# Optimization experiments

Measured on AMD Instinct MI355X. Metric: run time of the kernel, lower is better.

## Reference

```python
import jax, jax.numpy as jnp
import numpy as np

NUM_HEADS = 8
DIMS = 512
SR = 2
EPS = 1e-6


def setup_inputs() -> dict:
    key = jax.random.key(0)
    ks = jax.random.split(key, 12)
    B, H, W, C = 4, 64, 64, DIMS
    s = 0.02
    return {
        "x": jax.random.normal(ks[0], (B, H * W, C), dtype=jnp.float32),
        "Wq": jax.random.normal(ks[1], (C, DIMS), dtype=jnp.float32) * s,
        "bq": jnp.zeros((DIMS,), jnp.float32),
        "Wk": jax.random.normal(ks[2], (C, DIMS), dtype=jnp.float32) * s,
        "bk": jnp.zeros((DIMS,), jnp.float32),
        "Wv": jax.random.normal(ks[3], (C, DIMS), dtype=jnp.float32) * s,
        "bv": jnp.zeros((DIMS,), jnp.float32),
        "Wp": jax.random.normal(ks[4], (DIMS, DIMS), dtype=jnp.float32) * s,
        "bp": jnp.zeros((DIMS,), jnp.float32),
        "sr_w": jax.random.normal(ks[5], (SR, SR, C, DIMS), dtype=jnp.float32) * s,  # HWIO
        "sr_b": jnp.zeros((DIMS,), jnp.float32),
        "ln_g": jnp.ones((DIMS,), jnp.float32),
        "ln_b": jnp.zeros((DIMS,), jnp.float32),
        "H": 64,
        "W": 64,
    }


def reference(x, Wq, bq, Wk, bk, Wv, bv, Wp, bp, sr_w, sr_b, ln_g, ln_b, H, W):
    B, N, C = x.shape
    hd = DIMS // NUM_HEADS

    # spatial-reduction of K/V: strided conv (kernel=stride=SR, SAME) + LayerNorm
    kv = x.reshape(B, H, W, C)
    kv = jax.lax.conv_general_dilated(
        kv, sr_w, window_strides=(SR, SR), padding="SAME",
        dimension_numbers=("NHWC", "HWIO", "NHWC")) + sr_b
    kv = kv.reshape(B, -1, C)  # [B, Nk, C], Nk = (H//SR)*(W//SR)
    mu = jnp.mean(kv, axis=-1, keepdims=True)
    var = jnp.mean(jnp.square(kv - mu), axis=-1, keepdims=True)
    kv = (kv - mu) * jax.lax.rsqrt(var + EPS) * ln_g + ln_b
    Nk = kv.shape[1]

    # NOTE: original splits heads as reshape(B, N, head_dims, num_heads) and
    # indexes the LAST axis per head -> head h sees channels d*NUM_HEADS+h.
    q = (x @ Wq + bq).reshape(B, N, hd, NUM_HEADS)
    k = (kv @ Wk + bk).reshape(B, Nk, hd, NUM_HEADS)
    v = (kv @ Wv + bv).reshape(B, Nk, hd, NUM_HEADS)

    scores = jnp.einsum("bqdh,bkdh->bhqk", q, k) / jnp.sqrt(jnp.float32(hd))
    w = jax.nn.softmax(scores, axis=-1)
    # concat of heads along channels -> (B, N, NUM_HEADS, hd) layout
    out = jnp.einsum("bhqk,bkdh->bqhd", w, v).reshape(B, N, DIMS)
    return out @ Wp + bp
```

## Files before the change

### kernel.cpp

```cpp
#include <hip/hip_runtime.h>


typedef __attribute__((ext_vector_type(8))) _Float16 f16x8;
typedef __attribute__((ext_vector_type(4))) _Float16 f16x4;
typedef __attribute__((ext_vector_type(4))) float f32x4;

#define EXP2F(x) __builtin_amdgcn_exp2f(x)

__device__ __forceinline__ void gload_lds16(const _Float16* g, _Float16* l)
{
    __builtin_amdgcn_global_load_lds(
        (const __attribute__((address_space(1))) void*)g,
        (__attribute__((address_space(3))) void*)l, 16, 0, 0);
}

template<int N>
__device__ __forceinline__ void wait_vm()
{
    asm volatile("s_waitcnt vmcnt(%0)" :: "n"(N) : "memory");
}

__global__ __launch_bounds__(256)
void prep_k(const float* __restrict__ x,
            const float* __restrict__ Wq, const float* __restrict__ Wk,
            const float* __restrict__ Wv, const float* __restrict__ Wp,
            const float* __restrict__ srw,
            _Float16* __restrict__ xh, _Float16* __restrict__ wqt,
            _Float16* __restrict__ wkvt, _Float16* __restrict__ wpt,
            _Float16* __restrict__ srwt)
{
    __shared__ float T[32][33];
    const int id = blockIdx.x;
    const int t = threadIdx.x;

    if (id < 4096) {
        const size_t i = ((size_t)id * 256 + t) * 8;
        const float4 a = *(const float4*)(x + i);
        const float4 b = *(const float4*)(x + i + 4);
        f16x8 o;
        o[0] = (_Float16)a.x; o[1] = (_Float16)a.y; o[2] = (_Float16)a.z; o[3] = (_Float16)a.w;
        o[4] = (_Float16)b.x; o[5] = (_Float16)b.y; o[6] = (_Float16)b.z; o[7] = (_Float16)b.w;
        *(f16x8*)(xh + i) = o;
        return;
    }

    if (id < 5120) {
        const int id2 = id - 4096;
        const int z = id2 >> 8, k0 = ((id2 >> 4) & 15) * 32, n0 = (id2 & 15) * 32;
        const float* src; _Float16* dst; int perm;
        switch (z) {
            case 0:  src = Wq; dst = wqt;           perm = 1; break;
            case 1:  src = Wk; dst = wkvt;          perm = 1; break;
            case 2:  src = Wv; dst = wkvt + 262144; perm = 0; break;
            default: src = Wp; dst = wpt;           perm = 0; break;
        }
        {
            const int r = t >> 3, c = (t & 7) * 4;
            const float4 v = *(const float4*)(src + (size_t)(k0 + r) * 512 + n0 + c);
            T[r][c + 0] = v.x; T[r][c + 1] = v.y; T[r][c + 2] = v.z; T[r][c + 3] = v.w;
        }
        __syncthreads();
        {
            const int j = t >> 3, i0 = (t & 7) * 4;
            const int n = n0 + j;
            const int nper = perm ? ((n & 7) * 64 + (n >> 3)) : n;
            f16x4 o;
            o[0] = (_Float16)T[i0 + 0][j];
            o[1] = (_Float16)T[i0 + 1][j];
            o[2] = (_Float16)T[i0 + 2][j];
            o[3] = (_Float16)T[i0 + 3][j];
            *(f16x4*)(dst + (size_t)nper * 512 + k0 + i0) = o;
        }
        return;
    }

    {
        const int id3 = id - 5120;
        const int n0 = (id3 & 15) * 32, k0 = (id3 >> 4) * 32;
        {
            const int r = t >> 3, c = (t & 7) * 4;
            const float4 v = *(const float4*)(srw + (size_t)(k0 + r) * 512 + n0 + c);
            T[r][c + 0] = v.x; T[r][c + 1] = v.y; T[r][c + 2] = v.z; T[r][c + 3] = v.w;
        }
        __syncthreads();
        {
            const int j = t >> 3, i0 = (t & 7) * 4;
            f16x4 o;
            o[0] = (_Float16)T[i0 + 0][j];
            o[1] = (_Float16)T[i0 + 1][j];
            o[2] = (_Float16)T[i0 + 2][j];
            o[3] = (_Float16)T[i0 + 3][j];
            *(f16x4*)(srwt + (size_t)(n0 + j) * 2048 + k0 + i0) = o;
        }
        return;
    }
}

template<int MODE, bool CONV, int BM>
__device__ __forceinline__ void gemm_body(
    const int bx, const int by,
    const _Float16* __restrict__ A, const _Float16* __restrict__ Wt,
    const float* __restrict__ bias, const float* __restrict__ bias2,
    void* __restrict__ Cv, void* __restrict__ Cv2,
    _Float16* __restrict__ As, _Float16* __restrict__ Ws)
{
    constexpr int K = CONV ? 2048 : 512;
    constexpr int NIT = K / 32;
    constexpr int MT = BM / 32;
    constexpr int AI = BM / 64;
    constexpr int ABUF = BM * 32;
    constexpr int NBUF = (BM == 64) ? 4 : 3;
    constexpr int P = NBUF - 1;
    constexpr int L = AI + 2;
    const int tid = threadIdx.x;
    const int wave = tid >> 6, lane = tid & 63;
    const int quad = lane >> 4, l15 = lane & 15;
    const int wm = wave >> 1, wn = wave & 1;
    const int wrow = wm * (BM / 2);
    const int m0 = by * BM, n0 = bx * 128;

    const _Float16* abase[AI];
    int ac8[AI];
    #pragma unroll
    for (int t = 0; t < AI; ++t) {
        const int e = (wave * AI + t) * 64 + lane;
        const int row = e >> 2, c8 = (e & 3) * 8;
        ac8[t] = c8;
        if (CONV) {
            const int grow = m0 + row;
            const int b = grow >> 10, rem = grow & 1023;
            const int oh = rem >> 5, ow = rem & 31;
            abase[t] = A + ((size_t)((b * 64 + 2 * oh) * 64) + 2 * ow) * 512;
        } else {
            abase[t] = A + (size_t)(m0 + row) * K + c8;
        }
    }
    const _Float16* wbase[2];
    #pragma unroll
    for (int t = 0; t < 2; ++t) {
        const int e = (wave * 2 + t) * 64 + lane;
        const int row = e >> 2, c8 = (e & 3) * 8;
        wbase[t] = Wt + (size_t)(n0 + row) * K + c8;
    }

    auto stage = [&](const int k0, const int buf) {
        #pragma unroll
        for (int t = 0; t < AI; ++t) {
            const _Float16* gp;
            if (CONV) {
                const int gk = k0 + ac8[t];
                gp = abase[t] + ((gk >> 10) & 1) * 32768 + ((gk >> 9) & 1) * 512
                              + (gk & 511);
            } else {
                gp = abase[t] + k0;
            }
            gload_lds16(gp, &As[buf * ABUF + (wave * AI + t) * 512]);
        }
        #pragma unroll
        for (int t = 0; t < 2; ++t)
            gload_lds16(wbase[t] + k0, &Ws[buf * 4096 + (wave * 2 + t) * 512]);
    };

    f32x4 acc[MT][4] = {};

    #pragma unroll
    for (int p = 0; p < P; ++p) stage(p * 32, p);

    int cur = 0, nxt = P % NBUF;
    for (int it = 0; it < NIT; ++it) {
        int rem = NIT - 1 - it;
        if (rem > P - 1) rem = P - 1;
        switch (rem) {
            case 0:  wait_vm<0>(); break;
            case 1:  wait_vm<L>(); break;
            case 2:  wait_vm<2 * L>(); break;
            default: wait_vm<3 * L>(); break;
        }
        __builtin_amdgcn_s_barrier();
        __builtin_amdgcn_sched_barrier(0);
        if (it + P < NIT) {
            stage((it + P) * 32, nxt);
            nxt = (nxt + 1 == NBUF) ? 0 : nxt + 1;
        }

        f16x8 af[MT], bf[4];
        #pragma unroll
        for (int mt = 0; mt < MT; ++mt)
            af[mt] = *(const f16x8*)&As[cur * ABUF + (wrow + mt * 16 + l15) * 32 + quad * 8];
        #pragma unroll
        for (int nt = 0; nt < 4; ++nt)
            bf[nt] = *(const f16x8*)&Ws[cur * 4096 + (wn * 64 + nt * 16 + l15) * 32 + quad * 8];
        #pragma unroll
        for (int mt = 0; mt < MT; ++mt)
            #pragma unroll
            for (int nt = 0; nt < 4; ++nt)
                acc[mt][nt] = __builtin_amdgcn_mfma_f32_16x16x32_f16(
                    af[mt], bf[nt], acc[mt][nt], 0, 0, 0);

        cur = (cur + 1 == NBUF) ? 0 : cur + 1;
    }

    #pragma unroll
    for (int nt = 0; nt < 4; ++nt) {
        const int gcol = n0 + wn * 64 + nt * 16 + l15;
        float bv;
        if (MODE == 6) bv = bias[(gcol & 63) * 8 + (gcol >> 6)];
        else if (MODE == 5) bv = (gcol < 512) ? bias[(gcol & 63) * 8 + (gcol >> 6)]
                                              : bias2[gcol - 512];
        else bv = bias[gcol];
        #pragma unroll
        for (int mt = 0; mt < MT; ++mt) {
            const int row0 = m0 + wrow + mt * 16 + quad * 4;
            if (MODE == 0) {
                #pragma unroll
                for (int r = 0; r < 4; ++r)
                    ((float*)Cv)[(size_t)(row0 + r) * 512 + gcol] = acc[mt][nt][r] + bv;
            } else if (MODE == 4 || MODE == 6) {
                #pragma unroll
                for (int r = 0; r < 4; ++r)
                    ((_Float16*)Cv)[(size_t)(row0 + r) * 512 + gcol] =
                        (_Float16)(acc[mt][nt][r] + bv);
            } else {
                if (gcol < 512) {
                    #pragma unroll
                    for (int r = 0; r < 4; ++r)
                        ((_Float16*)Cv)[(size_t)(row0 + r) * 512 + gcol] =
                            (_Float16)(acc[mt][nt][r] + bv);
                } else {
                    const int c = gcol - 512;
                    const int h = c & 7, d = c >> 3;
                    const int b_ = row0 >> 10, jj = row0 & 1023;
                    f16x4 o;
                    #pragma unroll
                    for (int r = 0; r < 4; ++r) o[r] = (_Float16)(acc[mt][nt][r] + bv);
                    *(f16x4*)((_Float16*)Cv2 +
                              ((size_t)(b_ * 8 + h) * 64 + d) * 1024 + jj) = o;
                }
            }
        }
    }
}

template<int MODE, bool CONV, int BM>
__global__ __launch_bounds__(256)
void gemm_f16(const _Float16* __restrict__ A, const _Float16* __restrict__ Wt,
              const float* __restrict__ bias, const float* __restrict__ bias2,
              void* __restrict__ Cv, void* __restrict__ Cv2)
{
    __shared__ __align__(16) _Float16 lds[24576];
    constexpr int NBUF = (BM == 64) ? 4 : 3;
    gemm_body<MODE, CONV, BM>(blockIdx.x, blockIdx.y, A, Wt, bias, bias2,
                              Cv, Cv2, lds, lds + NBUF * BM * 32);
}

__global__ __launch_bounds__(256)
void convq_k(const _Float16* __restrict__ xh, const _Float16* __restrict__ srwt,
             const float* __restrict__ srb, const _Float16* __restrict__ wqt,
             const float* __restrict__ bq,
             _Float16* __restrict__ kvh, _Float16* __restrict__ qh)
{
    __shared__ __align__(16) _Float16 lds[24576];
    const int id = blockIdx.x;
    if (id < 256) {
        gemm_body<4, true, 64>(id & 3, id >> 2, xh, srwt, srb, nullptr,
                               kvh, nullptr, lds, lds + 4 * 64 * 32);
    } else {
        const int id2 = id - 256;
        gemm_body<6, false, 128>(id2 & 3, id2 >> 2, xh, wqt, bq, nullptr,
                                 qh, nullptr, lds, lds + 3 * 128 * 32);
    }
}

__global__ __launch_bounds__(256)
void ln_k(_Float16* __restrict__ buf, const float* __restrict__ g,
          const float* __restrict__ b)
{
    const int row = blockIdx.x;
    _Float16* p = buf + (size_t)row * 512;
    const int tid = threadIdx.x;
    const float vx = (float)p[tid * 2], vy = (float)p[tid * 2 + 1];
    float s = vx + vy, q = vx * vx + vy * vy;
    #pragma unroll
    for (int off = 32; off > 0; off >>= 1) {
        s += __shfl_xor(s, off);
        q += __shfl_xor(q, off);
    }
    __shared__ float ss[4], sq[4], stat[2];
    const int wid = tid >> 6;
    if ((tid & 63) == 0) { ss[wid] = s; sq[wid] = q; }
    __syncthreads();
    if (tid == 0) {
        const float S = ss[0] + ss[1] + ss[2] + ss[3];
        const float Q = sq[0] + sq[1] + sq[2] + sq[3];
        const float mu = S * (1.f / 512.f);
        const float var = fmaxf(Q * (1.f / 512.f) - mu * mu, 0.f);
        stat[0] = mu;
        stat[1] = rsqrtf(var + 1e-6f);
    }
    __syncthreads();
    const float mu = stat[0], rs = stat[1];
    const float2 gg = *(const float2*)(g + tid * 2);
    const float2 bb = *(const float2*)(b + tid * 2);
    p[tid * 2]     = (_Float16)((vx - mu) * rs * gg.x + bb.x);
    p[tid * 2 + 1] = (_Float16)((vy - mu) * rs * gg.y + bb.y);
}

__global__ __launch_bounds__(512)
void attn_mfma_k(const _Float16* __restrict__ qb,
                 const _Float16* __restrict__ kbuf,
                 const _Float16* __restrict__ vbuf,
                 _Float16* __restrict__ out)
{
    const int bh = blockIdx.y;
    const int qt = blockIdx.x;
    const int b = bh >> 3, h = bh & 7;
    const int tid = threadIdx.x;
    const int wave = tid >> 6, lane = tid & 63;
    const int quad = lane >> 4, l15 = lane & 15;

    __shared__ __align__(16) _Float16 Ks[2][64 * 72];
    __shared__ __align__(16) _Float16 Vs[2][64 * 72];

    const int qrow = b * 4096 + qt * 512 + wave * 64 + l15;
    const _Float16* qp = qb + (size_t)qrow * 512 + h * 64 + quad * 8;
    f16x8 qf[4][2];
    #pragma unroll
    for (int su = 0; su < 4; ++su) {
        qf[su][0] = *(const f16x8*)(qp + su * 16 * 512);
        qf[su][1] = *(const f16x8*)(qp + su * 16 * 512 + 32);
    }
    {
        const _Float16 qs = (_Float16)0.18033688f;
        #pragma unroll
        for (int su = 0; su < 4; ++su)
            #pragma unroll
            for (int g = 0; g < 2; ++g)
                #pragma unroll
                for (int i = 0; i < 8; ++i) qf[su][g][i] *= qs;
    }

    const int kr = tid >> 3, kc = (tid & 7) * 8;
    const int krp = (kr & 32) | ((kr & 4) << 2) | ((kr >> 1) & 12) | (kr & 3);
    const _Float16* kg = kbuf + (size_t)(b * 1024 + kr) * 512 + h * 64 + kc;
    const _Float16* vg = vbuf + (size_t)(bh * 64 + kr) * 1024 + kc;

    f16x8 krg = *(const f16x8*)kg;
    f16x8 vrg = *(const f16x8*)vg;
    *(f16x8*)&Ks[0][krp * 72 + kc] = krg;
    *(f16x8*)&Vs[0][kr * 72 + kc] = vrg;

    float l_run[4] = {0.f, 0.f, 0.f, 0.f};
    f32x4 acc[4][4] = {};

    for (int kt = 0; kt < 16; ++kt) {
        const int cur = kt & 1;
        __syncthreads();
        if (kt < 15) {
            krg = *(const f16x8*)(kg + (size_t)(kt + 1) * 64 * 512);
            vrg = *(const f16x8*)(vg + (kt + 1) * 64);
        }

        #pragma unroll
        for (int kb = 0; kb < 2; ++kb) {
            f16x8 pa[4];
            #pragma unroll
            for (int c = 0; c < 2; ++c) {
                const int ct = kb * 2 + c;
                const f16x8 kf0 = *(const f16x8*)&Ks[cur][(ct * 16 + l15) * 72 + quad * 8];
                const f16x8 kf1 = *(const f16x8*)&Ks[cur][(ct * 16 + l15) * 72 + 32 + quad * 8];
                #pragma unroll
                for (int su = 0; su < 4; ++su) {
                    f32x4 s = {};
                    s = __builtin_amdgcn_mfma_f32_16x16x32_f16(kf0, qf[su][0], s, 0, 0, 0);
                    s = __builtin_amdgcn_mfma_f32_16x16x32_f16(kf1, qf[su][1], s, 0, 0, 0);
                    const float p0 = EXP2F(s[0]), p1 = EXP2F(s[1]);
                    const float p2 = EXP2F(s[2]), p3 = EXP2F(s[3]);
                    l_run[su] += (p0 + p1) + (p2 + p3);
                    pa[su][c * 4 + 0] = (_Float16)p0;
                    pa[su][c * 4 + 1] = (_Float16)p1;
                    pa[su][c * 4 + 2] = (_Float16)p2;
                    pa[su][c * 4 + 3] = (_Float16)p3;
                }
            }
            __builtin_amdgcn_s_setprio(1);
            #pragma unroll
            for (int nt = 0; nt < 4; ++nt) {
                const f16x8 vf = *(const f16x8*)&Vs[cur][(nt * 16 + l15) * 72 + kb * 32 + quad * 8];
                #pragma unroll
                for (int su = 0; su < 4; ++su)
                    acc[su][nt] = __builtin_amdgcn_mfma_f32_16x16x32_f16(
                        pa[su], vf, acc[su][nt], 0, 0, 0);
            }
            __builtin_amdgcn_s_setprio(0);
        }

        if (kt < 15) {
            *(f16x8*)&Ks[cur ^ 1][krp * 72 + kc] = krg;
            *(f16x8*)&Vs[cur ^ 1][kr * 72 + kc] = vrg;
        }
    }

    #pragma unroll
    for (int su = 0; su < 4; ++su) {
        float ts = l_run[su];
        ts += __shfl_xor(ts, 16);
        ts += __shfl_xor(ts, 32);
        float inv[4];
        #pragma unroll
        for (int r = 0; r < 4; ++r)
            inv[r] = 1.0f / __shfl(ts, quad * 4 + r, 16);
        #pragma unroll
        for (int nt = 0; nt < 4; ++nt)
            #pragma unroll
            for (int r = 0; r < 4; ++r) {
                const int row = qt * 512 + wave * 64 + su * 16 + quad * 4 + r;
                const int col = h * 64 + nt * 16 + l15;
                out[((size_t)b * 4096 + row) * 512 + col] =
                    (_Float16)(acc[su][nt][r] * inv[r]);
            }
    }
}

extern "C" void kernel_launch(void* const* d_in, const int* in_sizes, int n_in,
                              void* d_out, int out_size, void* d_ws, size_t ws_size,
                              hipStream_t stream)
{
    const float* x   = (const float*)d_in[0];
    const float* Wq  = (const float*)d_in[1];
    const float* bq  = (const float*)d_in[2];
    const float* Wk  = (const float*)d_in[3];
    const float* bk  = (const float*)d_in[4];
    const float* Wv  = (const float*)d_in[5];
    const float* bv  = (const float*)d_in[6];
    const float* Wp  = (const float*)d_in[7];
    const float* bp  = (const float*)d_in[8];
    const float* srw = (const float*)d_in[9];
    const float* srb = (const float*)d_in[10];
    const float* lng = (const float*)d_in[11];
    const float* lnb = (const float*)d_in[12];

    _Float16* ws   = (_Float16*)d_ws;
    _Float16* xh   = ws;
    _Float16* atth = xh + 8388608;
    _Float16* kvh  = atth + 8388608;
    _Float16* kh   = kvh + 2097152;
    _Float16* vh   = kh + 2097152;
    _Float16* wqt  = vh + 2097152;
    _Float16* wkvt = wqt + 262144;
    _Float16* wpt  = wkvt + 524288;
    _Float16* srwt = wpt + 262144;
    _Float16* qh   = (_Float16*)d_out;

    prep_k<<<6144, 256, 0, stream>>>(x, Wq, Wk, Wv, Wp, srw,
                                     xh, wqt, wkvt, wpt, srwt);
    convq_k<<<768, 256, 0, stream>>>(xh, srwt, srb, wqt, bq, kvh, qh);
    ln_k<<<4096, 256, 0, stream>>>(kvh, lng, lnb);
    gemm_f16<5, false, 64><<<dim3(8, 64), 256, 0, stream>>>(
        kvh, wkvt, bk, bv, kh, vh);
    attn_mfma_k<<<dim3(8, 32), 512, 0, stream>>>(qh, kh, vh, atth);
    gemm_f16<0, false, 128><<<dim3(4, 128), 256, 0, stream>>>(
        atth, wpt, bp, nullptr, d_out, nullptr);
}
```

Measured before the change: 209.7 us.

## Halve attention block size and compute softmax row sums with MFMA

The attention kernel now runs 256-thread blocks covering 256 query rows, with twice as many blocks, so each thread loads two K and two V rows per tile. The row-sum of exponentials, formerly accumulated with VALU adds plus cross-lane shuffles, is now produced by an extra MFMA against a vector of ones. The aim is better occupancy and load balance across CUs and less VALU and shuffle work in the inner loop. In exchange, K/V tiles are reloaded by twice as many blocks and each inner step issues a few more MFMAs.

```diff
diff --git a/kernel.cpp b/kernel.cpp
--- a/kernel.cpp
+++ b/kernel.cpp
@@ -305,7 +305,7 @@
     p[tid * 2 + 1] = (_Float16)((vy - mu) * rs * gg.y + bb.y);
 }
 
-__global__ __launch_bounds__(512)
+__global__ __launch_bounds__(256)
 void attn_mfma_k(const _Float16* __restrict__ qb,
                  const _Float16* __restrict__ kbuf,
                  const _Float16* __restrict__ vbuf,
@@ -321,7 +321,7 @@
     __shared__ __align__(16) _Float16 Ks[2][64 * 72];
     __shared__ __align__(16) _Float16 Vs[2][64 * 72];
 
-    const int qrow = b * 4096 + qt * 512 + wave * 64 + l15;
+    const int qrow = b * 4096 + qt * 256 + wave * 64 + l15;
     const _Float16* qp = qb + (size_t)qrow * 512 + h * 64 + quad * 8;
     f16x8 qf[4][2];
     #pragma unroll
@@ -338,26 +338,37 @@
                 #pragma unroll
                 for (int i = 0; i < 8; ++i) qf[su][g][i] *= qs;
     }
+
+    f16x8 ones;
+    #pragma unroll
+    for (int i = 0; i < 8; ++i) ones[i] = (_Float16)1.0f;
 
     const int kr = tid >> 3, kc = (tid & 7) * 8;
     const int krp = (kr & 32) | ((kr & 4) << 2) | ((kr >> 1) & 12) | (kr & 3);
     const _Float16* kg = kbuf + (size_t)(b * 1024 + kr) * 512 + h * 64 + kc;
     const _Float16* vg = vbuf + (size_t)(bh * 64 + kr) * 1024 + kc;
 
-    f16x8 krg = *(const f16x8*)kg;
-    f16x8 vrg = *(const f16x8*)vg;
-    *(f16x8*)&Ks[0][krp * 72 + kc] = krg;
-    *(f16x8*)&Vs[0][kr * 72 + kc] = vrg;
-
-    float l_run[4] = {0.f, 0.f, 0.f, 0.f};
+    f16x8 krg0 = *(const f16x8*)kg;
+    f16x8 krg1 = *(const f16x8*)(kg + 32 * 512);
+    f16x8 vrg0 = *(const f16x8*)vg;
+    f16x8 vrg1 = *(const f16x8*)(vg + 32 * 1024);
+    *(f16x8*)&Ks[0][krp * 72 + kc] = krg0;
+    *(f16x8*)&Ks[0][(krp + 32) * 72 + kc] = krg1;
+    *(f16x8*)&Vs[0][kr * 72 + kc] = vrg0;
+    *(f16x8*)&Vs[0][(kr + 32) * 72 + kc] = vrg1;
+
     f32x4 acc[4][4] = {};
+    f32x4 acc_l[4] = {};
 
     for (int kt = 0; kt < 16; ++kt) {
         const int cur = kt & 1;
         __syncthreads();
         if (kt < 15) {
-            krg = *(const f16x8*)(kg + (size_t)(kt + 1) * 64 * 512);
-            vrg = *(const f16x8*)(vg + (kt + 1) * 64);
+            const size_t ko = (size_t)(kt + 1) * 64 * 512;
+            krg0 = *(const f16x8*)(kg + ko);
+            krg1 = *(const f16x8*)(kg + ko + 32 * 512);
+            vrg0 = *(const f16x8*)(vg + (kt + 1) * 64);
+            vrg1 = *(const f16x8*)(vg + (kt + 1) * 64 + 32 * 1024);
         }
 
         #pragma unroll
@@ -373,16 +384,17 @@
                     f32x4 s = {};
                     s = __builtin_amdgcn_mfma_f32_16x16x32_f16(kf0, qf[su][0], s, 0, 0, 0);
                     s = __builtin_amdgcn_mfma_f32_16x16x32_f16(kf1, qf[su][1], s, 0, 0, 0);
-                    const float p0 = EXP2F(s[0]), p1 = EXP2F(s[1]);
-                    const float p2 = EXP2F(s[2]), p3 = EXP2F(s[3]);
-                    l_run[su] += (p0 + p1) + (p2 + p3);
-                    pa[su][c * 4 + 0] = (_Float16)p0;
-                    pa[su][c * 4 + 1] = (_Float16)p1;
-                    pa[su][c * 4 + 2] = (_Float16)p2;
-                    pa[su][c * 4 + 3] = (_Float16)p3;
+                    pa[su][c * 4 + 0] = (_Float16)EXP2F(s[0]);
+                    pa[su][c * 4 + 1] = (_Float16)EXP2F(s[1]);
+                    pa[su][c * 4 + 2] = (_Float16)EXP2F(s[2]);
+                    pa[su][c * 4 + 3] = (_Float16)EXP2F(s[3]);
                 }
             }
             __builtin_amdgcn_s_setprio(1);
+            #pragma unroll
+            for (int su = 0; su < 4; ++su)
+                acc_l[su] = __builtin_amdgcn_mfma_f32_16x16x32_f16(
+                    pa[su], ones, acc_l[su], 0, 0, 0);
             #pragma unroll
             for (int nt = 0; nt < 4; ++nt) {
                 const f16x8 vf = *(const f16x8*)&Vs[cur][(nt * 16 + l15) * 72 + kb * 32 + quad * 8];
@@ -395,25 +407,23 @@
         }
 
         if (kt < 15) {
-            *(f16x8*)&Ks[cur ^ 1][krp * 72 + kc] = krg;
-            *(f16x8*)&Vs[cur ^ 1][kr * 72 + kc] = vrg;
+            *(f16x8*)&Ks[cur ^ 1][krp * 72 + kc] = krg0;
+            *(f16x8*)&Ks[cur ^ 1][(krp + 32) * 72 + kc] = krg1;
+            *(f16x8*)&Vs[cur ^ 1][kr * 72 + kc] = vrg0;
+            *(f16x8*)&Vs[cur ^ 1][(kr + 32) * 72 + kc] = vrg1;
         }
     }
 
     #pragma unroll
     for (int su = 0; su < 4; ++su) {
-        float ts = l_run[su];
-        ts += __shfl_xor(ts, 16);
-        ts += __shfl_xor(ts, 32);
         float inv[4];
         #pragma unroll
-        for (int r = 0; r < 4; ++r)
-            inv[r] = 1.0f / __shfl(ts, quad * 4 + r, 16);
+        for (int r = 0; r < 4; ++r) inv[r] = 1.0f / acc_l[su][r];
         #pragma unroll
         for (int nt = 0; nt < 4; ++nt)
             #pragma unroll
             for (int r = 0; r < 4; ++r) {
-                const int row = qt * 512 + wave * 64 + su * 16 + quad * 4 + r;
+                const int row = qt * 256 + wave * 64 + su * 16 + quad * 4 + r;
                 const int col = h * 64 + nt * 16 + l15;
                 out[((size_t)b * 4096 + row) * 512 + col] =
                     (_Float16)(acc[su][nt][r] * inv[r]);
@@ -457,7 +467,7 @@
     ln_k<<<4096, 256, 0, stream>>>(kvh, lng, lnb);
     gemm_f16<5, false, 64><<<dim3(8, 64), 256, 0, stream>>>(
         kvh, wkvt, bk, bv, kh, vh);
-    attn_mfma_k<<<dim3(8, 32), 512, 0, stream>>>(qh, kh, vh, atth);
+    attn_mfma_k<<<dim3(16, 32), 256, 0, stream>>>(qh, kh, vh, atth);
     gemm_f16<0, false, 128><<<dim3(4, 128), 256, 0, stream>>>(
         atth, wpt, bp, nullptr, d_out, nullptr);
 }
```

Result: slower. 223.4 us (+6.5%).
